# Kernel tuning notes

Hardware: AMD Instinct MI355X
Metric: run time of the kernel (lower is better)

The kernel has to match this reference:

```python
import jax, jax.numpy as jnp
import numpy as np

L, D, H, HD = 2, 2048, 16, 128          # layers, hidden, heads, head_dim
E, K, F, FS = 8, 2, 1408, 5632           # experts, top_k, moe_inter, shared_inter
V, T = 32000, 2048                       # vocab, tokens
EPS = 1e-6
ROPE_BASE = 1000000.0


def _rms(x, w):
    return x * jax.lax.rsqrt(jnp.mean(x * x, axis=-1, keepdims=True) + EPS) * w


def _rope(x, cos, sin):
    half = x.shape[-1] // 2
    x1, x2 = x[..., :half], x[..., half:]
    return jnp.concatenate([x1 * cos - x2 * sin, x1 * sin + x2 * cos], axis=-1)


def setup_inputs() -> dict:
    key = jax.random.key(0)
    ks = jax.random.split(key, 18)
    s = 0.02
    f = lambda k, shp: jax.random.normal(k, shp, jnp.float32) * s
    return {
        "input_ids": jax.random.randint(ks[0], (T,), 0, V, dtype=jnp.int32),
        "positions": jnp.arange(T, dtype=jnp.int32),
        "embed": f(ks[1], (V, D)),
        "qw": f(ks[2], (L, D, H * HD)),
        "kw": f(ks[3], (L, D, H * HD)),
        "vw": f(ks[4], (L, D, H * HD)),
        "ow": f(ks[5], (L, H * HD, D)),
        "ln1": jnp.ones((L, D), jnp.float32),
        "ln2": jnp.ones((L, D), jnp.float32),
        "router_w": f(ks[6], (L, D, E)),
        "sgate_w": f(ks[7], (L, D)),
        "wg": f(ks[8], (L, E, D, F)),
        "wu": f(ks[9], (L, E, D, F)),
        "wd": f(ks[10], (L, E, F, D)),
        "swg": f(ks[11], (L, D, FS)),
        "swu": f(ks[12], (L, D, FS)),
        "swd": f(ks[13], (L, FS, D)),
        "final_ln": jnp.ones((D,), jnp.float32),
    }


def _attn(x, positions, qw_l, kw_l, vw_l, ow_l):
    q = (x @ qw_l).reshape(T, H, HD)
    k = (x @ kw_l).reshape(T, H, HD)
    v = (x @ vw_l).reshape(T, H, HD)
    half = HD // 2
    inv = 1.0 / (ROPE_BASE ** (jnp.arange(half, dtype=jnp.float32) / half))
    ang = positions.astype(jnp.float32)[:, None] * inv[None, :]  # [T, half]
    cos, sin = jnp.cos(ang)[:, None, :], jnp.sin(ang)[:, None, :]
    q = _rope(q, cos, sin)
    k = _rope(k, cos, sin)
    scores = jnp.einsum('thd,shd->hts', q, k) * (HD ** -0.5)  # [H, T, T]
    mask = positions[:, None] >= positions[None, :]  # causal
    scores = jnp.where(mask[None], scores, -1e30)
    p = jax.nn.softmax(scores, axis=-1)
    o = jnp.einsum('hts,shd->thd', p, v).reshape(T, H * HD)
    return o @ ow_l


def _moe(x, router_w_l, sgate_w_l, wg_l, wu_l, wd_l, swg_l, swu_l, swd_l):
    # shared expert + its sigmoid gate
    sh = (jax.nn.silu(x @ swg_l) * (x @ swu_l)) @ swd_l
    sgate = jax.nn.sigmoid(x @ sgate_w_l)[:, None]
    # router: softmax in float32, then top-k with prob renorm (norm_topk_prob)
    probs = jax.nn.softmax((x @ router_w_l).astype(jnp.float32), axis=-1)
    topv, topi = jax.lax.top_k(probs, K)
    topv = topv / jnp.sum(topv, axis=-1, keepdims=True)
    combine = jnp.sum(jax.nn.one_hot(topi, E, dtype=x.dtype) * topv[..., None].astype(x.dtype), axis=1)  # [T, E]
    # dense grouped expert FFN, combined by routing weights (scatter-add equivalent)
    g = jnp.einsum('td,edf->etf', x, wg_l)
    u = jnp.einsum('td,edf->etf', x, wu_l)
    y = jnp.einsum('etf,efd->etd', jax.nn.silu(g) * u, wd_l)
    moe_out = jnp.einsum('te,etd->td', combine, y)
    return (moe_out + sgate * sh) * (1.0 / K ** 0.5)


def reference(input_ids, positions, embed, qw, kw, vw, ow, ln1, ln2, router_w,
              sgate_w, wg, wu, wd, swg, swu, swd, final_ln):
    h = embed[input_ids]  # [T, D]
    residual = None
    for l in range(L):
        if residual is None:
            residual = h
            x = _rms(h, ln1[l])
        else:
            residual = h + residual
            x = _rms(residual, ln1[l])
        h = _attn(x, positions, qw[l], kw[l], vw[l], ow[l])
        residual = h + residual
        x = _rms(residual, ln2[l])
        h = _moe(x, router_w[l], sgate_w[l], wg[l], wu[l], wd[l], swg[l], swu[l], swd[l])
    residual = h + residual
    return _rms(residual, final_ln)
```

## Files before the change

### kernel.cpp

```cpp
#include <hip/hip_runtime.h>
#include <stdint.h>

#define TT 2048
#define DD 2048
#define HH 16
#define HDIM 128
#define NE 8
#define TOPK 2
#define FF 1408
#define FSS 5632
#define NL 2

typedef __bf16 bf16;
typedef __bf16 bf16x2 __attribute__((ext_vector_type(2)));
typedef __bf16 bf16x4 __attribute__((ext_vector_type(4)));
typedef __bf16 bf16x8 __attribute__((ext_vector_type(8)));
typedef float f32x4 __attribute__((ext_vector_type(4)));

__device__ __forceinline__ void split1(float f, bf16& h, bf16& l) {
  bf16 hb = (bf16)f;
  h = hb;
  l = (bf16)(f - (float)hb);
}

__device__ __forceinline__ void gload16(const void* g, void* l) {
  __builtin_amdgcn_global_load_lds((const __attribute__((address_space(1))) void*)g,
                                   (__attribute__((address_space(3))) void*)l, 16, 0, 0);
}

template<bool LO>
__launch_bounds__(256)
__global__ void k_wtrans(const float* __restrict__ W, bf16* __restrict__ Wh,
                         bf16* __restrict__ Wl, int Kd, int N)
{
  __shared__ float T[64][68];
  const size_t slab = (size_t)blockIdx.z * (size_t)Kd * (size_t)N;
  const float* Wp = W + slab;
  const int k0 = blockIdx.x * 64, n0 = blockIdx.y * 64;
  const int tid = threadIdx.x;
  const int rr = tid >> 2, c4 = (tid & 3) * 4;
  const float* src = Wp + (size_t)(k0 + rr) * N + n0 + c4;
#pragma unroll
  for (int j = 0; j < 4; ++j) {
    f32x4 v = *(const f32x4*)(src + j * 16);
    *(f32x4*)&T[rr][c4 + j * 16] = v;
  }
  __syncthreads();
  const int nn = tid >> 2, kk = (tid & 3) * 16;
  bf16x8 h0, h1, l0, l1;
#pragma unroll
  for (int j = 0; j < 8; ++j) {
    bf16 hb, lb;
    split1(T[kk + j][nn], hb, lb);
    h0[j] = hb; l0[j] = lb;
    split1(T[kk + 8 + j][nn], hb, lb);
    h1[j] = hb; l1[j] = lb;
  }
  size_t out = slab + (size_t)(n0 + nn) * Kd + k0 + kk;
  *(bf16x8*)&Wh[out] = h0;
  *(bf16x8*)&Wh[out + 8] = h1;
  if (LO) {
    *(bf16x8*)&Wl[out] = l0;
    *(bf16x8*)&Wl[out + 8] = l1;
  }
}

template<int BMT, int NT, bool EXPERT, bool GATHER, int OM>
__launch_bounds__(256, (BMT == 128 ? 3 : 4))
__global__ void k_gemmp(const bf16* __restrict__ Ah, const bf16* __restrict__ Al,
                        const bf16* __restrict__ Bh, const bf16* __restrict__ Bl,
                        void* __restrict__ C1, void* __restrict__ C2,
                        int M, int N, int Kd, int lda, int ldc,
                        const int* __restrict__ perm, const int* __restrict__ cnt,
                        const int* __restrict__ ofs)
{
  constexpr int PL = (NT == 3) ? 2 : 1;
  constexpr int ASUB = BMT / 16;
  constexpr int AISS = PL * ASUB;
  constexpr int BISS = PL * 8;
  constexpr int QPW = (AISS + BISS) / 4;
  constexpr int IF = BMT / 32;

  int m_count = M, row_base = 0;
  size_t boff = 0;
  if (EXPERT) {
    int e = blockIdx.z;
    m_count = cnt[e];
    if ((int)(blockIdx.x * BMT) >= m_count) return;
    row_base = ofs[e];
    boff = (size_t)e * (size_t)N * (size_t)Kd;
  }
  const int tid = threadIdx.x, lane = tid & 63, wid = tid >> 6;
  const int wm = (wid >> 1) * (BMT / 2), wn = (wid & 1) * 64;
  const int lr = lane & 15, g = lane >> 4;
  const int n0 = blockIdx.y * 128;
  const int m0 = blockIdx.x * BMT;

  __shared__ bf16 As[PL][BMT][32];
  __shared__ bf16 Bs[PL][128][32];

  const bf16* srcp[QPW];
#pragma unroll
  for (int j = 0; j < QPW; ++j) {
    int q = wid * QPW + j;
    int r16 = lane >> 2, kc = lane & 3;
    if (q < AISS) {
      int pl = q / ASUB, sub = q % ASUB;
      int r = sub * 16 + r16;
      int tok;
      if (EXPERT) {
        int lrow = m0 + r;
        if (lrow >= m_count) lrow = m_count - 1;
        tok = GATHER ? perm[row_base + lrow] : (row_base + lrow);
      } else {
        tok = m0 + r;
      }
      const bf16* base = (pl == 0) ? Ah : Al;
      srcp[j] = base + (size_t)tok * lda + kc * 8;
    } else {
      int qb = q - AISS;
      int pl = qb >> 3, sub = qb & 7;
      int nrow = sub * 16 + r16;
      const bf16* base = (pl == 0) ? Bh : Bl;
      srcp[j] = base + boff + (size_t)(n0 + nrow) * Kd + kc * 8;
    }
  }

  f32x4 acc[IF][4];
#pragma unroll
  for (int i = 0; i < IF; ++i)
#pragma unroll
    for (int j = 0; j < 4; ++j)
      acc[i][j] = (f32x4){0.f, 0.f, 0.f, 0.f};

  auto ISSUE = [&](int k0) {
#pragma unroll
    for (int j = 0; j < QPW; ++j) {
      int q = wid * QPW + j;
      bf16* dst;
      if (q < AISS) {
        int pl = q / ASUB, sub = q % ASUB;
        dst = &As[pl][sub * 16][0];
      } else {
        int qb = q - AISS;
        int pl = qb >> 3, sub = qb & 7;
        dst = &Bs[pl][sub * 16][0];
      }
      gload16(srcp[j] + k0, dst);
    }
  };

  const int NTk = Kd >> 5;
  ISSUE(0);
  for (int t = 0; t < NTk; ++t) {
    __syncthreads();
    bf16x8 bfr[4][PL], afr[IF][PL];
#pragma unroll
    for (int jj = 0; jj < 4; ++jj)
#pragma unroll
      for (int pl = 0; pl < PL; ++pl)
        bfr[jj][pl] = *(const bf16x8*)&Bs[pl][wn + jj * 16 + lr][g * 8];
#pragma unroll
    for (int i = 0; i < IF; ++i)
#pragma unroll
      for (int pl = 0; pl < PL; ++pl)
        afr[i][pl] = *(const bf16x8*)&As[pl][wm + i * 16 + lr][g * 8];
    __syncthreads();
    if (t + 1 < NTk) ISSUE((t + 1) << 5);
#pragma unroll
    for (int i = 0; i < IF; ++i)
#pragma unroll
      for (int jj = 0; jj < 4; ++jj) {
        f32x4 a2 = acc[i][jj];
        a2 = __builtin_amdgcn_mfma_f32_16x16x32_bf16(afr[i][0], bfr[jj][0], a2, 0, 0, 0);
        if (NT == 3) {
          a2 = __builtin_amdgcn_mfma_f32_16x16x32_bf16(afr[i][0], bfr[jj][1], a2, 0, 0, 0);
          a2 = __builtin_amdgcn_mfma_f32_16x16x32_bf16(afr[i][1], bfr[jj][0], a2, 0, 0, 0);
        }
        acc[i][jj] = a2;
      }
  }

  const int r0 = g * 4;
#pragma unroll
  for (int i = 0; i < IF; ++i) {
    int lrow0 = m0 + wm + i * 16 + r0;
#pragma unroll
    for (int j = 0; j < 4; ++j) {
      int col = n0 + wn + j * 16 + lr;
      if (OM == 4) {
        bf16x4 ph, pl;
#pragma unroll
        for (int r = 0; r < 4; ++r) { bf16 hb, lb; split1(acc[i][j][r], hb, lb); ph[r] = hb; pl[r] = lb; }
        *(bf16x4*)&((bf16*)C1)[(size_t)col * ldc + lrow0] = ph;
        *(bf16x4*)&((bf16*)C2)[(size_t)col * ldc + lrow0] = pl;
      } else {
#pragma unroll
        for (int r = 0; r < 4; ++r) {
          int lrow = lrow0 + r;
          if (EXPERT && lrow >= m_count) continue;
          size_t off = (size_t)(row_base + lrow) * ldc + col;
          if (OM == 1) {
            ((float*)C1)[off] = acc[i][j][r];
          } else {
            bf16 hb, lb; split1(acc[i][j][r], hb, lb);
            ((bf16*)C1)[off] = hb;
            ((bf16*)C2)[off] = lb;
          }
        }
      }
    }
  }
}

__launch_bounds__(256)
__global__ void k_attns(const bf16* __restrict__ Qh, const bf16* __restrict__ Ql,
                        const bf16* __restrict__ Kh, const bf16* __restrict__ Kl,
                        const bf16* __restrict__ Vh, const bf16* __restrict__ Vl,
                        bf16* __restrict__ Oh, bf16* __restrict__ Ol)
{
  const int tid = threadIdx.x;
  const int lane = tid & 63, wid = tid >> 6;
  const int head = blockIdx.y;
  const int qbase = (gridDim.x - 1 - blockIdx.x) * 16;
  const int lr = lane & 15, g = lane >> 4;

  __shared__ float o_l[4][16][132];
  __shared__ float m_l[4][16], l_l[4][16];
  bf16* plbase = (bf16*)&o_l[0][0][0];
  bf16 (*pl_h)[40] = (bf16(*)[40])(plbase + wid * 16 * 40);
  bf16 (*pl_l)[40] = (bf16(*)[40])(plbase + (4 + wid) * 16 * 40);

  bf16x8 qfh[4], qfl[4];
  {
    size_t qoff = (size_t)(qbase + lr) * DD + head * HDIM;
#pragma unroll
    for (int c = 0; c < 4; ++c) {
      qfh[c] = *(const bf16x8*)(Qh + qoff + c * 32 + g * 8);
      qfl[c] = *(const bf16x8*)(Ql + qoff + c * 32 + g * 8);
    }
  }

  f32x4 o[8];
#pragma unroll
  for (int d = 0; d < 8; ++d) o[d] = (f32x4){0.f, 0.f, 0.f, 0.f};
  float m_r[4] = {-1e30f, -1e30f, -1e30f, -1e30f};
  float l_r[4] = {0.f, 0.f, 0.f, 0.f};

  const int qend = qbase + 16;
  for (int kb = wid * 32; kb < qend; kb += 128) {
    f32x4 s0 = {0.f,0.f,0.f,0.f}, s1 = {0.f,0.f,0.f,0.f};
    size_t k0off = (size_t)(kb + lr) * DD + head * HDIM;
    size_t k1off = k0off + (size_t)16 * DD;
#pragma unroll
    for (int c = 0; c < 4; ++c) {
      bf16x8 kh = *(const bf16x8*)(Kh + k0off + c * 32 + g * 8);
      bf16x8 kl = *(const bf16x8*)(Kl + k0off + c * 32 + g * 8);
      s0 = __builtin_amdgcn_mfma_f32_16x16x32_bf16(qfh[c], kh, s0, 0, 0, 0);
      s0 = __builtin_amdgcn_mfma_f32_16x16x32_bf16(qfh[c], kl, s0, 0, 0, 0);
      s0 = __builtin_amdgcn_mfma_f32_16x16x32_bf16(qfl[c], kh, s0, 0, 0, 0);
    }
#pragma unroll
    for (int c = 0; c < 4; ++c) {
      bf16x8 kh = *(const bf16x8*)(Kh + k1off + c * 32 + g * 8);
      bf16x8 kl = *(const bf16x8*)(Kl + k1off + c * 32 + g * 8);
      s1 = __builtin_amdgcn_mfma_f32_16x16x32_bf16(qfh[c], kh, s1, 0, 0, 0);
      s1 = __builtin_amdgcn_mfma_f32_16x16x32_bf16(qfh[c], kl, s1, 0, 0, 0);
      s1 = __builtin_amdgcn_mfma_f32_16x16x32_bf16(qfl[c], kh, s1, 0, 0, 0);
    }
    float p0[4], p1[4], mx[4], alpha[4];
#pragma unroll
    for (int r = 0; r < 4; ++r) {
      int q = qbase + g * 4 + r;
      float a0 = s0[r] * 0.08838834764831845f;
      float a1 = s1[r] * 0.08838834764831845f;
      if (kb + lr > q)      a0 = -1e30f;
      if (kb + 16 + lr > q) a1 = -1e30f;
      p0[r] = a0; p1[r] = a1;
      mx[r] = fmaxf(a0, a1);
    }
#pragma unroll
    for (int off = 1; off < 16; off <<= 1)
#pragma unroll
      for (int r = 0; r < 4; ++r) mx[r] = fmaxf(mx[r], __shfl_xor(mx[r], off, 64));
#pragma unroll
    for (int r = 0; r < 4; ++r) {
      float mn = fmaxf(m_r[r], mx[r]);
      alpha[r] = __expf(m_r[r] - mn);
      m_r[r] = mn;
      p0[r] = __expf(p0[r] - mn);
      p1[r] = __expf(p1[r] - mn);
    }
    float ps[4];
#pragma unroll
    for (int r = 0; r < 4; ++r) ps[r] = p0[r] + p1[r];
#pragma unroll
    for (int off = 1; off < 16; off <<= 1)
#pragma unroll
      for (int r = 0; r < 4; ++r) ps[r] += __shfl_xor(ps[r], off, 64);
#pragma unroll
    for (int r = 0; r < 4; ++r) l_r[r] = l_r[r] * alpha[r] + ps[r];
#pragma unroll
    for (int d = 0; d < 8; ++d)
#pragma unroll
      for (int r = 0; r < 4; ++r) o[d][r] *= alpha[r];
#pragma unroll
    for (int r = 0; r < 4; ++r) {
      bf16 hb, lb;
      split1(p0[r], hb, lb);
      pl_h[g * 4 + r][lr] = hb;
      pl_l[g * 4 + r][lr] = lb;
      split1(p1[r], hb, lb);
      pl_h[g * 4 + r][16 + lr] = hb;
      pl_l[g * 4 + r][16 + lr] = lb;
    }
    bf16x8 pah = *(const bf16x8*)&pl_h[lr][g * 8];
    bf16x8 pal = *(const bf16x8*)&pl_l[lr][g * 8];
#pragma unroll
    for (int d = 0; d < 8; ++d) {
      size_t voff = (size_t)(head * HDIM + d * 16 + lr) * TT + kb + g * 8;
      bf16x8 vfh = *(const bf16x8*)(Vh + voff);
      bf16x8 vfl = *(const bf16x8*)(Vl + voff);
      o[d] = __builtin_amdgcn_mfma_f32_16x16x32_bf16(pah, vfh, o[d], 0, 0, 0);
      o[d] = __builtin_amdgcn_mfma_f32_16x16x32_bf16(pah, vfl, o[d], 0, 0, 0);
      o[d] = __builtin_amdgcn_mfma_f32_16x16x32_bf16(pal, vfh, o[d], 0, 0, 0);
    }
  }

  __syncthreads();
  if (lr == 0) {
#pragma unroll
    for (int r = 0; r < 4; ++r) {
      m_l[wid][g * 4 + r] = m_r[r];
      l_l[wid][g * 4 + r] = l_r[r];
    }
  }
#pragma unroll
  for (int d = 0; d < 8; ++d)
#pragma unroll
    for (int r = 0; r < 4; ++r)
      o_l[wid][g * 4 + r][d * 16 + lr] = o[d][r];
  __syncthreads();

  const int row = tid >> 4;
  const int c0 = (tid & 15) * 8;
  float m0v = m_l[0][row], m1v = m_l[1][row], m2v = m_l[2][row], m3v = m_l[3][row];
  float ms = fmaxf(fmaxf(m0v, m1v), fmaxf(m2v, m3v));
  float s0v = __expf(m0v - ms), s1v = __expf(m1v - ms);
  float s2v = __expf(m2v - ms), s3v = __expf(m3v - ms);
  float lsum = l_l[0][row] * s0v + l_l[1][row] * s1v
             + l_l[2][row] * s2v + l_l[3][row] * s3v;
  float inv = 1.f / lsum;
  union { bf16 b[8]; uint4 u; } ph, pl;
#pragma unroll
  for (int j = 0; j < 8; ++j) {
    float v = o_l[0][row][c0 + j] * s0v + o_l[1][row][c0 + j] * s1v
            + o_l[2][row][c0 + j] * s2v + o_l[3][row][c0 + j] * s3v;
    bf16 hb, lb;
    split1(v * inv, hb, lb);
    ph.b[j] = hb; pl.b[j] = lb;
  }
  size_t oi = (size_t)(qbase + row) * DD + head * HDIM + c0;
  *(uint4*)(Oh + oi) = ph.u;
  *(uint4*)(Ol + oi) = pl.u;
}

__global__ void k_embed(const int* __restrict__ ids, const float* __restrict__ Em,
                        float* __restrict__ Hout)
{
  int t = blockIdx.x, tid = threadIdx.x;
  const float4* s = (const float4*)(Em + (size_t)ids[t] * DD);
  float4* dst = (float4*)(Hout + (size_t)t * DD);
  dst[tid] = s[tid];
  dst[tid + 256] = s[tid + 256];
}

template<bool ADDIN, bool WF32, bool FINAL>
__launch_bounds__(256)
__global__ void k_addrms(const float* __restrict__ Hin, float* __restrict__ Res,
                         const float* __restrict__ W,
                         bf16* __restrict__ Xh, bf16* __restrict__ Xl,
                         float* __restrict__ Xf)
{
  const int t = blockIdx.x, tid = threadIdx.x;
  const size_t base = (size_t)t * DD + tid * 8;
  float x[8];
  {
    const float4* hp = (const float4*)(Hin + base);
    float4 a = hp[0], b = hp[1];
    x[0]=a.x; x[1]=a.y; x[2]=a.z; x[3]=a.w;
    x[4]=b.x; x[5]=b.y; x[6]=b.z; x[7]=b.w;
    if (ADDIN) {
      const float4* rp = (const float4*)(Res + base);
      float4 c = rp[0], d = rp[1];
      x[0]+=c.x; x[1]+=c.y; x[2]+=c.z; x[3]+=c.w;
      x[4]+=d.x; x[5]+=d.y; x[6]+=d.z; x[7]+=d.w;
    }
  }
  {
    float4* rp = (float4*)(Res + base);
    rp[0] = make_float4(x[0], x[1], x[2], x[3]);
    rp[1] = make_float4(x[4], x[5], x[6], x[7]);
  }
  float ss = 0.f;
#pragma unroll
  for (int j = 0; j < 8; ++j) ss += x[j] * x[j];
#pragma unroll
  for (int off = 32; off; off >>= 1) ss += __shfl_xor(ss, off, 64);
  __shared__ float red[4];
  if ((tid & 63) == 0) red[tid >> 6] = ss;
  __syncthreads();
  float tot = red[0] + red[1] + red[2] + red[3];
  float sc = rsqrtf(tot * (1.0f / DD) + 1e-6f);
  float y[8];
#pragma unroll
  for (int j = 0; j < 8; ++j) y[j] = x[j] * sc * W[tid * 8 + j];
  if (!FINAL) {
    union { bf16 b[8]; uint4 u; } ph, pl;
#pragma unroll
    for (int j = 0; j < 8; ++j) { bf16 hb, lb; split1(y[j], hb, lb); ph.b[j] = hb; pl.b[j] = lb; }
    *(uint4*)(Xh + base) = ph.u;
    *(uint4*)(Xl + base) = pl.u;
  }
  if (WF32 || FINAL) {
    float4* xp = (float4*)(Xf + base);
    xp[0] = make_float4(y[0], y[1], y[2], y[3]);
    xp[1] = make_float4(y[4], y[5], y[6], y[7]);
  }
}

__global__ void k_rope2(bf16* __restrict__ Qh, bf16* __restrict__ Ql,
                        bf16* __restrict__ Kh, bf16* __restrict__ Kl,
                        const int* __restrict__ pos)
{
  int idx = blockIdx.x * 256 + threadIdx.x;
  int d = idx & 63;
  int h = (idx >> 6) & (HH - 1);
  int t = idx >> 10;
  if (t >= TT) return;
  double inv = pow(1.0e6, -(double)d / 64.0);
  double ang = (double)pos[t] * inv;
  double sd, cd;
  sincos(ang, &sd, &cd);
  float sn = (float)sd, cs = (float)cd;
  size_t base = (size_t)t * DD + h * HDIM + d;
  float q1 = (float)Qh[base] + (float)Ql[base];
  float q2 = (float)Qh[base + 64] + (float)Ql[base + 64];
  float qa = q1 * cs - q2 * sn, qb = q1 * sn + q2 * cs;
  bf16 hb, lb;
  split1(qa, hb, lb); Qh[base] = hb;      Ql[base] = lb;
  split1(qb, hb, lb); Qh[base + 64] = hb; Ql[base + 64] = lb;
  float k1 = (float)Kh[base] + (float)Kl[base];
  float k2 = (float)Kh[base + 64] + (float)Kl[base + 64];
  float ka = k1 * cs - k2 * sn, kb2 = k1 * sn + k2 * cs;
  split1(ka, hb, lb);  Kh[base] = hb;      Kl[base] = lb;
  split1(kb2, hb, lb); Kh[base + 64] = hb; Kl[base + 64] = lb;
}

__launch_bounds__(64)
__global__ void k_router(const float* __restrict__ Xf, const float* __restrict__ RW,
                         const float* __restrict__ SGW, int* __restrict__ eidx,
                         float* __restrict__ ew, float* __restrict__ sgate,
                         int* __restrict__ cnt)
{
  const int t = blockIdx.x, lane = threadIdx.x;
  const float* x = Xf + (size_t)t * DD;
  float acc[8] = {0,0,0,0,0,0,0,0};
  float sg = 0.f;
  for (int i = lane; i < DD; i += 64) {
    float xv = x[i];
    const float4* w = (const float4*)(RW + (size_t)i * NE);
    float4 w0 = w[0], w1 = w[1];
    acc[0] += xv * w0.x; acc[1] += xv * w0.y; acc[2] += xv * w0.z; acc[3] += xv * w0.w;
    acc[4] += xv * w1.x; acc[5] += xv * w1.y; acc[6] += xv * w1.z; acc[7] += xv * w1.w;
    sg += xv * SGW[i];
  }
#pragma unroll
  for (int off = 32; off; off >>= 1) {
#pragma unroll
    for (int e = 0; e < 8; ++e) acc[e] += __shfl_xor(acc[e], off, 64);
    sg += __shfl_xor(sg, off, 64);
  }
  if (lane == 0) {
    int i0 = 0; float v0 = acc[0];
    for (int e = 1; e < 8; ++e) if (acc[e] > v0) { v0 = acc[e]; i0 = e; }
    int i1 = -1; float v1 = -1e30f;
    for (int e = 0; e < 8; ++e) if (e != i0 && acc[e] > v1) { v1 = acc[e]; i1 = e; }
    float w0 = 1.f / (1.f + expf(v1 - v0));
    eidx[2*t] = i0; eidx[2*t+1] = i1;
    ew[2*t] = w0; ew[2*t+1] = 1.f - w0;
    sgate[t] = 1.f / (1.f + expf(-sg));
    atomicAdd(&cnt[i0], 1);
    atomicAdd(&cnt[i1], 1);
  }
}

__global__ void k_scan(const int* __restrict__ cnt, int* __restrict__ ofs)
{
  if (threadIdx.x == 0) {
    int s = 0;
    for (int e = 0; e < NE; ++e) { ofs[e] = s; s += cnt[e]; }
    ofs[NE] = s;
  }
}

__global__ void k_assign(const int* __restrict__ eidx, const int* __restrict__ ofs,
                         int* __restrict__ cursor, int* __restrict__ perm,
                         int* __restrict__ posof)
{
  int t = blockIdx.x * 256 + threadIdx.x;
  if (t >= TT) return;
#pragma unroll
  for (int j = 0; j < 2; ++j) {
    int e = eidx[2*t + j];
    int p = ofs[e] + atomicAdd(&cursor[e], 1);
    perm[p] = t;
    posof[2*t + j] = p;
  }
}

__global__ void k_silup(const float* __restrict__ G, const float* __restrict__ U,
                        bf16* __restrict__ H, bf16* __restrict__ L)
{
  int i = (blockIdx.x * 256 + threadIdx.x) * 4;
  float4 g = *(const float4*)(G + i);
  float4 u = *(const float4*)(U + i);
  float s[4];
  s[0] = g.x / (1.f + expf(-g.x)) * u.x;
  s[1] = g.y / (1.f + expf(-g.y)) * u.y;
  s[2] = g.z / (1.f + expf(-g.z)) * u.z;
  s[3] = g.w / (1.f + expf(-g.w)) * u.w;
  bf16x4 h, l;
#pragma unroll
  for (int j = 0; j < 4; ++j) { bf16 hb, lb; split1(s[j], hb, lb); h[j] = hb; l[j] = lb; }
  *(bf16x4*)(H + i) = h;
  *(bf16x4*)(L + i) = l;
}

__global__ void k_combine(const float* __restrict__ Y, const float* __restrict__ SH,
                          const float* __restrict__ sgate, const float* __restrict__ ew,
                          const int* __restrict__ posof, float* __restrict__ Hout)
{
  int t = blockIdx.x, tid = threadIdx.x;
  int p0 = posof[2*t], p1 = posof[2*t+1];
  float w0 = ew[2*t], w1 = ew[2*t+1];
  float sgv = sgate[t];
  int d0 = tid * 8;
  const float4* a = (const float4*)(Y + (size_t)p0 * DD + d0);
  const float4* b = (const float4*)(Y + (size_t)p1 * DD + d0);
  float4 a0 = a[0], a1 = a[1], b0 = b[0], b1 = b[1];
  float y0[8] = {a0.x,a0.y,a0.z,a0.w,a1.x,a1.y,a1.z,a1.w};
  float y1[8] = {b0.x,b0.y,b0.z,b0.w,b1.x,b1.y,b1.z,b1.w};
  const float4* shp = (const float4*)(SH + (size_t)t * DD + d0);
  float4 sa = shp[0], sb = shp[1];
  float shv[8] = {sa.x, sa.y, sa.z, sa.w, sb.x, sb.y, sb.z, sb.w};
  float out[8];
#pragma unroll
  for (int j = 0; j < 8; ++j)
    out[j] = (y0[j] * w0 + y1[j] * w1 + sgv * shv[j]) * 0.70710678118654752f;
  float4* op = (float4*)(Hout + (size_t)t * DD + d0);
  op[0] = make_float4(out[0], out[1], out[2], out[3]);
  op[1] = make_float4(out[4], out[5], out[6], out[7]);
}

extern "C" void kernel_launch(void* const* d_in, const int* in_sizes, int n_in,
                              void* d_out, int out_size, void* d_ws, size_t ws_size,
                              hipStream_t stream)
{
  (void)in_sizes; (void)n_in; (void)out_size; (void)ws_size;
  const int*   ids  = (const int*)d_in[0];
  const int*   pos  = (const int*)d_in[1];
  const float* emb  = (const float*)d_in[2];
  const float* qw   = (const float*)d_in[3];
  const float* kw   = (const float*)d_in[4];
  const float* vw   = (const float*)d_in[5];
  const float* ow   = (const float*)d_in[6];
  const float* ln1  = (const float*)d_in[7];
  const float* ln2  = (const float*)d_in[8];
  const float* rw   = (const float*)d_in[9];
  const float* sgw  = (const float*)d_in[10];
  const float* wg   = (const float*)d_in[11];
  const float* wu   = (const float*)d_in[12];
  const float* wd   = (const float*)d_in[13];
  const float* swg  = (const float*)d_in[14];
  const float* swu  = (const float*)d_in[15];
  const float* swd  = (const float*)d_in[16];
  const float* fln  = (const float*)d_in[17];

  char* p = (char*)d_ws;
  auto alloc = [&](size_t b) { char* r = p; p += (b + 255) & ~(size_t)255; return r; };

  const size_t TD = (size_t)TT * DD;
  float* resid = (float*)alloc(TD * 4);
  float* hbuf  = (float*)alloc(TD * 4);
  float* xf    = (float*)alloc(TD * 4);
  bf16*  xh    = (bf16*) alloc(TD * 2);
  bf16*  xl    = (bf16*) alloc(TD * 2);
  bf16*  qhb   = (bf16*) alloc(TD * 2);
  bf16*  qlb   = (bf16*) alloc(TD * 2);
  bf16*  khb   = (bf16*) alloc(TD * 2);
  bf16*  klb   = (bf16*) alloc(TD * 2);
  bf16*  vth   = (bf16*) alloc(TD * 2);
  bf16*  vtl   = (bf16*) alloc(TD * 2);
  bf16*  aoh   = (bf16*) alloc(TD * 2);
  bf16*  aol   = (bf16*) alloc(TD * 2);
  float* shb   = (float*)alloc(TD * 4);
  const size_t SGF = (size_t)TT * FSS;
  const size_t GEF = (size_t)TT * TOPK * FF;
  bf16*  shph  = (bf16*) alloc(SGF * 2);
  bf16*  shpl  = (bf16*) alloc(SGF * 2);
  bf16*  geph  = (bf16*) alloc(GEF * 2);
  bf16*  gepl  = (bf16*) alloc(GEF * 2);
  float* region = (float*)alloc(2 * SGF * 4);
  float* sgbf = region;
  float* subf = region + SGF;
  float* gebf = region;
  float* uebf = region + GEF;
  float* ybf  = region + 2 * GEF;
  const size_t WME = (size_t)NE * DD * FF;
  bf16* wbh = (bf16*)alloc(WME * 2);
  bf16* wbl = (bf16*)alloc(WME * 2);
  int*   eidx  = (int*)  alloc((size_t)TT * TOPK * 4);
  float* ewb   = (float*)alloc((size_t)TT * TOPK * 4);
  float* sgate = (float*)alloc((size_t)TT * 4);
  int*   perm  = (int*)  alloc((size_t)TT * TOPK * 4);
  int*   posof = (int*)  alloc((size_t)TT * TOPK * 4);
  int*   cnt   = (int*)  alloc(64);
  int*   ofs   = (int*)  alloc(64);
  int*   cursor = cnt + 8;

  k_embed<<<TT, 256, 0, stream>>>(ids, emb, hbuf);

  for (int l = 0; l < NL; ++l) {
    const float* qw_l  = qw  + (size_t)l * DD * DD;
    const float* kw_l  = kw  + (size_t)l * DD * DD;
    const float* vw_l  = vw  + (size_t)l * DD * DD;
    const float* ow_l  = ow  + (size_t)l * DD * DD;
    const float* ln1_l = ln1 + (size_t)l * DD;
    const float* ln2_l = ln2 + (size_t)l * DD;
    const float* rw_l  = rw  + (size_t)l * DD * NE;
    const float* sgw_l = sgw + (size_t)l * DD;
    const float* wg_l  = wg  + (size_t)l * NE * DD * FF;
    const float* wu_l  = wu  + (size_t)l * NE * DD * FF;
    const float* wd_l  = wd  + (size_t)l * NE * FF * DD;
    const float* swg_l = swg + (size_t)l * DD * FSS;
    const float* swu_l = swu + (size_t)l * DD * FSS;
    const float* swd_l = swd + (size_t)l * FSS * DD;
    const bool last = (l == NL - 1);

    if (l == 0)
      k_addrms<false,false,false><<<TT,256,0,stream>>>(hbuf, resid, ln1_l, xh, xl, nullptr);
    else
      k_addrms<true, false,false><<<TT,256,0,stream>>>(hbuf, resid, ln1_l, xh, xl, nullptr);

    k_wtrans<true><<<dim3(32,32),256,0,stream>>>(qw_l, wbh, wbl, DD, DD);
    k_gemmp<64,3,false,false,3><<<dim3(32,16),256,0,stream>>>(xh, xl, wbh, wbl, qhb, qlb, TT, DD, DD, DD, DD, nullptr,nullptr,nullptr);
    k_wtrans<true><<<dim3(32,32),256,0,stream>>>(kw_l, wbh, wbl, DD, DD);
    k_gemmp<64,3,false,false,3><<<dim3(32,16),256,0,stream>>>(xh, xl, wbh, wbl, khb, klb, TT, DD, DD, DD, DD, nullptr,nullptr,nullptr);
    k_wtrans<true><<<dim3(32,32),256,0,stream>>>(vw_l, wbh, wbl, DD, DD);
    k_gemmp<64,3,false,false,4><<<dim3(32,16),256,0,stream>>>(xh, xl, wbh, wbl, vth, vtl, TT, DD, DD, DD, TT, nullptr,nullptr,nullptr);
    k_rope2<<<(TT*HH*64)/256, 256, 0, stream>>>(qhb, qlb, khb, klb, pos);
    k_attns<<<dim3(TT/16, HH), 256, 0, stream>>>(qhb, qlb, khb, klb, vth, vtl, aoh, aol);
    k_wtrans<true><<<dim3(32,32),256,0,stream>>>(ow_l, wbh, wbl, DD, DD);
    k_gemmp<64,3,false,false,1><<<dim3(32,16),256,0,stream>>>(aoh, aol, wbh, wbl, hbuf, nullptr, TT, DD, DD, DD, DD, nullptr,nullptr,nullptr);

    k_addrms<true,true,false><<<TT,256,0,stream>>>(hbuf, resid, ln2_l, xh, xl, xf);

    hipMemsetAsync(cnt, 0, 64, stream);
    k_router<<<TT, 64, 0, stream>>>(xf, rw_l, sgw_l, eidx, ewb, sgate, cnt);
    k_scan<<<1, 64, 0, stream>>>(cnt, ofs);
    k_assign<<<TT/256, 256, 0, stream>>>(eidx, ofs, cursor, perm, posof);

    if (!last) {
      k_wtrans<true><<<dim3(32,88),256,0,stream>>>(swg_l, wbh, wbl, DD, FSS);
      k_gemmp<128,3,false,false,1><<<dim3(16,44),256,0,stream>>>(xh, xl, wbh, wbl, sgbf, nullptr, TT, FSS, DD, DD, FSS, nullptr,nullptr,nullptr);
      k_wtrans<true><<<dim3(32,88),256,0,stream>>>(swu_l, wbh, wbl, DD, FSS);
      k_gemmp<128,3,false,false,1><<<dim3(16,44),256,0,stream>>>(xh, xl, wbh, wbl, subf, nullptr, TT, FSS, DD, DD, FSS, nullptr,nullptr,nullptr);
      k_silup<<<(TT*FSS/4)/256, 256, 0, stream>>>(sgbf, subf, shph, shpl);
      k_wtrans<true><<<dim3(88,32),256,0,stream>>>(swd_l, wbh, wbl, FSS, DD);
      k_gemmp<64,3,false,false,1><<<dim3(32,16),256,0,stream>>>(shph, shpl, wbh, wbl, shb, nullptr, TT, DD, FSS, FSS, DD, nullptr,nullptr,nullptr);
    } else {
      k_wtrans<false><<<dim3(32,88),256,0,stream>>>(swg_l, wbh, wbl, DD, FSS);
      k_gemmp<128,1,false,false,1><<<dim3(16,44),256,0,stream>>>(xh, xl, wbh, wbl, sgbf, nullptr, TT, FSS, DD, DD, FSS, nullptr,nullptr,nullptr);
      k_wtrans<false><<<dim3(32,88),256,0,stream>>>(swu_l, wbh, wbl, DD, FSS);
      k_gemmp<128,1,false,false,1><<<dim3(16,44),256,0,stream>>>(xh, xl, wbh, wbl, subf, nullptr, TT, FSS, DD, DD, FSS, nullptr,nullptr,nullptr);
      k_silup<<<(TT*FSS/4)/256, 256, 0, stream>>>(sgbf, subf, shph, shpl);
      k_wtrans<false><<<dim3(88,32),256,0,stream>>>(swd_l, wbh, wbl, FSS, DD);
      k_gemmp<64,1,false,false,1><<<dim3(32,16),256,0,stream>>>(shph, shpl, wbh, wbl, shb, nullptr, TT, DD, FSS, FSS, DD, nullptr,nullptr,nullptr);
    }

    if (!last) {
      k_wtrans<true><<<dim3(32,22,NE),256,0,stream>>>(wg_l, wbh, wbl, DD, FF);
      k_gemmp<64,3,true,true,1><<<dim3(64,11,NE),256,0,stream>>>(xh, xl, wbh, wbl, gebf, nullptr, TT, FF, DD, DD, FF, perm, cnt, ofs);
      k_wtrans<true><<<dim3(32,22,NE),256,0,stream>>>(wu_l, wbh, wbl, DD, FF);
      k_gemmp<64,3,true,true,1><<<dim3(64,11,NE),256,0,stream>>>(xh, xl, wbh, wbl, uebf, nullptr, TT, FF, DD, DD, FF, perm, cnt, ofs);
      k_silup<<<(GEF/4)/256, 256, 0, stream>>>(gebf, uebf, geph, gepl);
      k_wtrans<true><<<dim3(22,32,NE),256,0,stream>>>(wd_l, wbh, wbl, FF, DD);
      k_gemmp<64,3,true,false,1><<<dim3(64,16,NE),256,0,stream>>>(geph, gepl, wbh, wbl, ybf, nullptr, TT, DD, FF, FF, DD, nullptr, cnt, ofs);
    } else {
      k_wtrans<false><<<dim3(32,22,NE),256,0,stream>>>(wg_l, wbh, wbl, DD, FF);
      k_gemmp<64,1,true,true,1><<<dim3(64,11,NE),256,0,stream>>>(xh, xl, wbh, wbl, gebf, nullptr, TT, FF, DD, DD, FF, perm, cnt, ofs);
      k_wtrans<false><<<dim3(32,22,NE),256,0,stream>>>(wu_l, wbh, wbl, DD, FF);
      k_gemmp<64,1,true,true,1><<<dim3(64,11,NE),256,0,stream>>>(xh, xl, wbh, wbl, uebf, nullptr, TT, FF, DD, DD, FF, perm, cnt, ofs);
      k_silup<<<(GEF/4)/256, 256, 0, stream>>>(gebf, uebf, geph, gepl);
      k_wtrans<false><<<dim3(22,32,NE),256,0,stream>>>(wd_l, wbh, wbl, FF, DD);
      k_gemmp<64,1,true,false,1><<<dim3(64,16,NE),256,0,stream>>>(geph, gepl, wbh, wbl, ybf, nullptr, TT, DD, FF, FF, DD, nullptr, cnt, ofs);
    }
    k_combine<<<TT, 256, 0, stream>>>(ybf, shb, sgate, ewb, posof, hbuf);
  }

  k_addrms<true,false,true><<<TT,256,0,stream>>>(hbuf, resid, fln, nullptr, nullptr, (float*)d_out);
}
```

Measured before the change: 3.947 ms.

## Swizzle GEMM shared-memory tiles and transpose attention score MFMA operands

```diff
diff --git a/kernel.cpp b/kernel.cpp
--- a/kernel.cpp
+++ b/kernel.cpp
@@ -103,7 +103,8 @@
 #pragma unroll
   for (int j = 0; j < QPW; ++j) {
     int q = wid * QPW + j;
-    int r16 = lane >> 2, kc = lane & 3;
+    int r16 = lane >> 2;
+    int kc = (lane & 3) ^ ((lane >> 3) & 3);
     if (q < AISS) {
       int pl = q / ASUB, sub = q % ASUB;
       int r = sub * 16 + r16;
@@ -150,6 +151,7 @@
     }
   };
 
+  const int gs = (g ^ ((lr >> 1) & 3)) * 8;
   const int NTk = Kd >> 5;
   ISSUE(0);
   for (int t = 0; t < NTk; ++t) {
@@ -159,12 +161,12 @@
     for (int jj = 0; jj < 4; ++jj)
 #pragma unroll
       for (int pl = 0; pl < PL; ++pl)
-        bfr[jj][pl] = *(const bf16x8*)&Bs[pl][wn + jj * 16 + lr][g * 8];
+        bfr[jj][pl] = *(const bf16x8*)&Bs[pl][wn + jj * 16 + lr][gs];
 #pragma unroll
     for (int i = 0; i < IF; ++i)
 #pragma unroll
       for (int pl = 0; pl < PL; ++pl)
-        afr[i][pl] = *(const bf16x8*)&As[pl][wm + i * 16 + lr][g * 8];
+        afr[i][pl] = *(const bf16x8*)&As[pl][wm + i * 16 + lr][gs];
     __syncthreads();
     if (t + 1 < NTk) ISSUE((t + 1) << 5);
 #pragma unroll
@@ -244,8 +246,7 @@
   f32x4 o[8];
 #pragma unroll
   for (int d = 0; d < 8; ++d) o[d] = (f32x4){0.f, 0.f, 0.f, 0.f};
-  float m_r[4] = {-1e30f, -1e30f, -1e30f, -1e30f};
-  float l_r[4] = {0.f, 0.f, 0.f, 0.f};
+  float m_r = -1e30f, l_r = 0.f;
 
   const int qend = qbase + 16;
   for (int kb = wid * 32; kb < qend; kb += 128) {
@@ -256,63 +257,62 @@
     for (int c = 0; c < 4; ++c) {
       bf16x8 kh = *(const bf16x8*)(Kh + k0off + c * 32 + g * 8);
       bf16x8 kl = *(const bf16x8*)(Kl + k0off + c * 32 + g * 8);
-      s0 = __builtin_amdgcn_mfma_f32_16x16x32_bf16(qfh[c], kh, s0, 0, 0, 0);
-      s0 = __builtin_amdgcn_mfma_f32_16x16x32_bf16(qfh[c], kl, s0, 0, 0, 0);
-      s0 = __builtin_amdgcn_mfma_f32_16x16x32_bf16(qfl[c], kh, s0, 0, 0, 0);
+      s0 = __builtin_amdgcn_mfma_f32_16x16x32_bf16(kh, qfh[c], s0, 0, 0, 0);
+      s0 = __builtin_amdgcn_mfma_f32_16x16x32_bf16(kl, qfh[c], s0, 0, 0, 0);
+      s0 = __builtin_amdgcn_mfma_f32_16x16x32_bf16(kh, qfl[c], s0, 0, 0, 0);
     }
 #pragma unroll
     for (int c = 0; c < 4; ++c) {
       bf16x8 kh = *(const bf16x8*)(Kh + k1off + c * 32 + g * 8);
       bf16x8 kl = *(const bf16x8*)(Kl + k1off + c * 32 + g * 8);
-      s1 = __builtin_amdgcn_mfma_f32_16x16x32_bf16(qfh[c], kh, s1, 0, 0, 0);
-      s1 = __builtin_amdgcn_mfma_f32_16x16x32_bf16(qfh[c], kl, s1, 0, 0, 0);
-      s1 = __builtin_amdgcn_mfma_f32_16x16x32_bf16(qfl[c], kh, s1, 0, 0, 0);
-    }
-    float p0[4], p1[4], mx[4], alpha[4];
+      s1 = __builtin_amdgcn_mfma_f32_16x16x32_bf16(kh, qfh[c], s1, 0, 0, 0);
+      s1 = __builtin_amdgcn_mfma_f32_16x16x32_bf16(kl, qfh[c], s1, 0, 0, 0);
+      s1 = __builtin_amdgcn_mfma_f32_16x16x32_bf16(kh, qfl[c], s1, 0, 0, 0);
+    }
+    float p0[4], p1[4];
+    float mloc = -1e30f;
+    const int q = qbase + lr;
 #pragma unroll
     for (int r = 0; r < 4; ++r) {
-      int q = qbase + g * 4 + r;
+      int k0i = kb + g * 4 + r;
       float a0 = s0[r] * 0.08838834764831845f;
       float a1 = s1[r] * 0.08838834764831845f;
-      if (kb + lr > q)      a0 = -1e30f;
-      if (kb + 16 + lr > q) a1 = -1e30f;
+      if (k0i > q)      a0 = -1e30f;
+      if (k0i + 16 > q) a1 = -1e30f;
       p0[r] = a0; p1[r] = a1;
-      mx[r] = fmaxf(a0, a1);
-    }
-#pragma unroll
-    for (int off = 1; off < 16; off <<= 1)
-#pragma unroll
-      for (int r = 0; r < 4; ++r) mx[r] = fmaxf(mx[r], __shfl_xor(mx[r], off, 64));
+      mloc = fmaxf(mloc, fmaxf(a0, a1));
+    }
+    mloc = fmaxf(mloc, __shfl_xor(mloc, 16, 64));
+    mloc = fmaxf(mloc, __shfl_xor(mloc, 32, 64));
+    float mn = fmaxf(m_r, mloc);
+    float alpha = __expf(m_r - mn);
+    m_r = mn;
+    float ps = 0.f;
 #pragma unroll
     for (int r = 0; r < 4; ++r) {
-      float mn = fmaxf(m_r[r], mx[r]);
-      alpha[r] = __expf(m_r[r] - mn);
-      m_r[r] = mn;
       p0[r] = __expf(p0[r] - mn);
       p1[r] = __expf(p1[r] - mn);
-    }
-    float ps[4];
-#pragma unroll
-    for (int r = 0; r < 4; ++r) ps[r] = p0[r] + p1[r];
-#pragma unroll
-    for (int off = 1; off < 16; off <<= 1)
-#pragma unroll
-      for (int r = 0; r < 4; ++r) ps[r] += __shfl_xor(ps[r], off, 64);
-#pragma unroll
-    for (int r = 0; r < 4; ++r) l_r[r] = l_r[r] * alpha[r] + ps[r];
+      ps += p0[r] + p1[r];
+    }
+    ps += __shfl_xor(ps, 16, 64);
+    ps += __shfl_xor(ps, 32, 64);
+    l_r = l_r * alpha + ps;
+    float alr[4];
+#pragma unroll
+    for (int r = 0; r < 4; ++r) alr[r] = __shfl(alpha, g * 4 + r, 64);
 #pragma unroll
     for (int d = 0; d < 8; ++d)
 #pragma unroll
-      for (int r = 0; r < 4; ++r) o[d][r] *= alpha[r];
+      for (int r = 0; r < 4; ++r) o[d][r] *= alr[r];
 #pragma unroll
     for (int r = 0; r < 4; ++r) {
       bf16 hb, lb;
       split1(p0[r], hb, lb);
-      pl_h[g * 4 + r][lr] = hb;
-      pl_l[g * 4 + r][lr] = lb;
+      pl_h[lr][g * 4 + r] = hb;
+      pl_l[lr][g * 4 + r] = lb;
       split1(p1[r], hb, lb);
-      pl_h[g * 4 + r][16 + lr] = hb;
-      pl_l[g * 4 + r][16 + lr] = lb;
+      pl_h[lr][16 + g * 4 + r] = hb;
+      pl_l[lr][16 + g * 4 + r] = lb;
     }
     bf16x8 pah = *(const bf16x8*)&pl_h[lr][g * 8];
     bf16x8 pal = *(const bf16x8*)&pl_l[lr][g * 8];
@@ -328,12 +328,9 @@
   }
 
   __syncthreads();
-  if (lr == 0) {
-#pragma unroll
-    for (int r = 0; r < 4; ++r) {
-      m_l[wid][g * 4 + r] = m_r[r];
-      l_l[wid][g * 4 + r] = l_r[r];
-    }
+  if (g == 0) {
+    m_l[wid][lr] = m_r;
+    l_l[wid][lr] = l_r;
   }
 #pragma unroll
   for (int d = 0; d < 8; ++d)
```

Result: no change. 3.952 ms (+0.1%).
